# Kernel tuning notes

Measured on AMD Instinct MI355X. Metric: run time of the kernel, lower is better.

## Reference

```python
import jax, jax.numpy as jnp
import numpy as np

S, E, H, D, F = 2048, 1280, 16, 80, 5120
EPS = 1e-6


def _ln(x, g, b):
    m = x.mean(-1, keepdims=True)
    v = x.var(-1, keepdims=True)
    return (x - m) * jax.lax.rsqrt(v + EPS) * g + b


def _rotate_half(x):
    x1, x2 = jnp.split(x, 2, axis=-1)
    return jnp.concatenate([-x2, x1], axis=-1)


def _quick_gelu(x):
    return x * jax.nn.sigmoid(1.702 * x)


def setup_inputs() -> dict:
    key = jax.random.key(0)
    ks = jax.random.split(key, 12)
    inp = {
        "hidden_states": jax.random.normal(ks[0], (S, E), jnp.float32),
        "attention_mask": jnp.ones((1, 1, S, S), jnp.bool_),
        "cos": jax.random.uniform(ks[1], (S, D), jnp.float32),
        "sin": jax.random.uniform(ks[2], (S, D), jnp.float32),
        "ln1_g": jnp.ones((E,), jnp.float32),
        "ln1_b": jnp.zeros((E,), jnp.float32),
        "ln2_g": jnp.ones((E,), jnp.float32),
        "ln2_b": jnp.zeros((E,), jnp.float32),
        "w_qkv": jax.random.normal(ks[3], (E, 3 * E), jnp.float32) * (E ** -0.5),
        "b_qkv": jax.random.normal(ks[4], (3 * E,), jnp.float32) * 0.02,
        "w_o": jax.random.normal(ks[5], (E, E), jnp.float32) * (E ** -0.5),
        "b_o": jax.random.normal(ks[6], (E,), jnp.float32) * 0.02,
        "w_fc1": jax.random.normal(ks[7], (E, F), jnp.float32) * (E ** -0.5),
        "b_fc1": jax.random.normal(ks[8], (F,), jnp.float32) * 0.02,
        "w_fc2": jax.random.normal(ks[9], (F, E), jnp.float32) * (F ** -0.5),
        "b_fc2": jax.random.normal(ks[10], (E,), jnp.float32) * 0.02,
    }
    return inp


def reference(hidden_states, attention_mask, cos, sin, ln1_g, ln1_b, ln2_g, ln2_b,
              w_qkv, b_qkv, w_o, b_o, w_fc1, b_fc1, w_fc2, b_fc2):
    x = hidden_states  # [S, E]
    h = _ln(x, ln1_g, ln1_b)
    qkv = h @ w_qkv + b_qkv  # [S, 3E]
    q, k, v = jnp.split(qkv, 3, axis=-1)
    q = q.reshape(S, H, D)
    k = k.reshape(S, H, D)
    v = v.reshape(S, H, D)
    # rotary in fp32, cos/sin broadcast over head axis: [S, 1, D]
    c = cos[:, None, :].astype(jnp.float32)
    s = sin[:, None, :].astype(jnp.float32)
    qf, kf = q.astype(jnp.float32), k.astype(jnp.float32)
    q = (qf * c + _rotate_half(qf) * s).astype(q.dtype)
    k = (kf * c + _rotate_half(kf) * s).astype(k.dtype)
    # attention scores [H, S, S]
    scores = jnp.einsum('shd,thd->hst', q, k) / np.float32(np.sqrt(D))
    scores = jnp.where(attention_mask[0], scores, jnp.finfo(scores.dtype).min)
    probs = jax.nn.softmax(scores.astype(jnp.float32), axis=-1).astype(q.dtype)
    attn = jnp.einsum('hst,thd->shd', probs, v).reshape(S, E)
    attn = attn @ w_o + b_o
    x = x + attn
    h2 = _ln(x, ln2_g, ln2_b)
    mlp = _quick_gelu(h2 @ w_fc1 + b_fc1) @ w_fc2 + b_fc2
    return x + mlp
```

## Files before the change

kernel.cpp:

```cpp
#include <hip/hip_runtime.h>
#include <stdint.h>
#include <math.h>

#define S_LEN 2048
#define EMB   1280
#define NHEAD 16
#define HDIM  80
#define FDIM  5120

typedef __bf16 bf16x8 __attribute__((ext_vector_type(8)));
typedef float  f32x4  __attribute__((ext_vector_type(4)));
typedef int    i32x4  __attribute__((ext_vector_type(4)));
typedef unsigned short u16x8 __attribute__((ext_vector_type(8)));
typedef unsigned short u16x4 __attribute__((ext_vector_type(4)));

__device__ __forceinline__ float b2f(unsigned short u) {
    union { float f; unsigned int i; } x; x.i = ((unsigned int)u) << 16; return x.f;
}
__device__ __forceinline__ unsigned short f2b(float f) {
    union { float f; unsigned int i; } x; x.f = f;
    unsigned int r = x.i + 0x7FFFu + ((x.i >> 16) & 1u);
    return (unsigned short)(r >> 16);
}

__device__ __forceinline__ float wave_rsum(float v) {
    #pragma unroll
    for (int o = 32; o; o >>= 1) v += __shfl_down(v, o);
    return v;
}

__device__ __forceinline__ void trans64(
    const float* __restrict__ in, unsigned short* __restrict__ out,
    int R, int C, int bx, int by, int tid)
{
    __shared__ unsigned short tile[64][68];
    int c0 = bx * 64, r0 = by * 64;
    #pragma unroll
    for (int p = 0; p < 4; ++p) {
        int row  = p * 16 + (tid >> 4);
        int col4 = (tid & 15) * 4;
        f32x4 v = *(const f32x4*)&in[(size_t)(r0 + row) * C + c0 + col4];
        u16x4 b;
        #pragma unroll
        for (int j = 0; j < 4; ++j) b[j] = f2b(v[j]);
        *(u16x4*)&tile[row][col4] = b;
    }
    __syncthreads();
    #pragma unroll
    for (int p = 0; p < 4; ++p) {
        int orow = p * 16 + (tid >> 4);
        int oc4  = (tid & 15) * 4;
        u16x4 v;
        #pragma unroll
        for (int j = 0; j < 4; ++j) v[j] = tile[oc4 + j][orow];
        *(u16x4*)&out[(size_t)(c0 + orow) * R + r0 + oc4] = v;
    }
}

__global__ __launch_bounds__(256) void transpose4_kernel(
    const float* __restrict__ w_qkv, unsigned short* __restrict__ wT_qkv,
    const float* __restrict__ w_o,   unsigned short* __restrict__ wT_o,
    const float* __restrict__ w_fc1, unsigned short* __restrict__ wT_fc1,
    const float* __restrict__ w_fc2, unsigned short* __restrict__ wT_fc2)
{
    int id = blockIdx.x, tid = threadIdx.x;
    if (id < 1200) {
        trans64(w_qkv, wT_qkv, 1280, 3840, id % 60, id / 60, tid);
    } else if (id < 1600) {
        int t = id - 1200;
        trans64(w_o, wT_o, 1280, 1280, t % 20, t / 20, tid);
    } else if (id < 3200) {
        int t = id - 1600;
        trans64(w_fc1, wT_fc1, 1280, 5120, t % 80, t / 80, tid);
    } else {
        int t = id - 3200;
        trans64(w_fc2, wT_fc2, 5120, 1280, t % 20, t / 20, tid);
    }
}

__global__ __launch_bounds__(256) void ln_kernel(
    const float* __restrict__ x,
    const float* __restrict__ g,
    const float* __restrict__ b,
    unsigned short* __restrict__ out)
{
    int row = blockIdx.x, tid = threadIdx.x;
    int lane = tid & 63, wave = tid >> 6;
    const float* xr = x + (size_t)row * EMB;
    float v[5], s = 0.f, ss = 0.f;
    #pragma unroll
    for (int i = 0; i < 5; ++i) {
        float f = xr[tid + i * 256];
        v[i] = f; s += f; ss += f * f;
    }
    s = wave_rsum(s); ss = wave_rsum(ss);
    __shared__ float rs[4], rss[4];
    if (lane == 0) { rs[wave] = s; rss[wave] = ss; }
    __syncthreads();
    float st  = rs[0] + rs[1] + rs[2] + rs[3];
    float sst = rss[0] + rss[1] + rss[2] + rss[3];
    float mean = st * (1.0f / EMB);
    float var  = sst * (1.0f / EMB) - mean * mean;
    float inv  = rsqrtf(var + 1e-6f);
    unsigned short* orow = out + (size_t)row * EMB;
    #pragma unroll
    for (int i = 0; i < 5; ++i) {
        int c = tid + i * 256;
        orow[c] = f2b((v[i] - mean) * inv * g[c] + b[c]);
    }
}

__global__ __launch_bounds__(256) void reduce2ln_kernel(
    const float* __restrict__ part,
    const float* __restrict__ res,
    const float* __restrict__ bias,
    const float* __restrict__ g,
    const float* __restrict__ b,
    float* __restrict__ x_out,
    unsigned short* __restrict__ h_out)
{
    int row = blockIdx.x, tid = threadIdx.x;
    int lane = tid & 63, wave = tid >> 6;
    const size_t slice = (size_t)S_LEN * EMB;
    const float* p0 = part + (size_t)row * EMB;
    const float* p1 = p0 + slice;
    const float* rr = res + (size_t)row * EMB;
    float v[5], s = 0.f, ss = 0.f;
    #pragma unroll
    for (int i = 0; i < 5; ++i) {
        int c = tid + i * 256;
        float f = rr[c] + bias[c] + p0[c] + p1[c];
        v[i] = f; s += f; ss += f * f;
    }
    s = wave_rsum(s); ss = wave_rsum(ss);
    __shared__ float rs[4], rss[4];
    if (lane == 0) { rs[wave] = s; rss[wave] = ss; }
    __syncthreads();
    float st  = rs[0] + rs[1] + rs[2] + rs[3];
    float sst = rss[0] + rss[1] + rss[2] + rss[3];
    float mean = st * (1.0f / EMB);
    float var  = sst * (1.0f / EMB) - mean * mean;
    float inv  = rsqrtf(var + 1e-6f);
    float* xrow = x_out + (size_t)row * EMB;
    unsigned short* hrow = h_out + (size_t)row * EMB;
    #pragma unroll
    for (int i = 0; i < 5; ++i) {
        int c = tid + i * 256;
        xrow[c] = v[i];
        hrow[c] = f2b((v[i] - mean) * inv * g[c] + b[c]);
    }
}

template<int Z>
__global__ __launch_bounds__(256) void reduceZ_kernel(
    const float* __restrict__ part,
    const float* __restrict__ res,
    const float* __restrict__ bias,
    float* __restrict__ out)
{
    size_t i4 = ((size_t)blockIdx.x * 256 + threadIdx.x) * 4;
    int colb = (int)(i4 % EMB);
    f32x4 a = *(const f32x4*)&res[i4];
    f32x4 bv = *(const f32x4*)&bias[colb];
    a += bv;
    const size_t slice = (size_t)S_LEN * EMB;
    #pragma unroll
    for (int z = 0; z < Z; ++z)
        a += *(const f32x4*)&part[z * slice + i4];
    *(f32x4*)&out[i4] = a;
}

template<int EPI, int OM, int SPLIT, int BN>
__global__ __launch_bounds__(256) void gemm_kernel(
    const unsigned short* __restrict__ A,
    const unsigned short* __restrict__ Bt,
    const float* __restrict__ bias,
    void* __restrict__ Cv,
    int M, int N, int K)
{
    constexpr int NI = BN / 32;
    constexpr bool BX = (BN > 128);
    __shared__ __align__(16) unsigned short As[2][128 * 32];
    __shared__ __align__(16) unsigned short Bs[2][BN * 32];

    int tid = threadIdx.x;
    int lane = tid & 63, wave = tid >> 6;

    int gx = gridDim.x, gy = gridDim.y;
    int nwg = gx * gy * gridDim.z;
    int flat = blockIdx.x + gx * (blockIdx.y + gy * blockIdx.z);
    int cpx = nwg >> 3;
    int logical = (flat & 7) * cpx + (flat >> 3);
    int bx = logical % gx;
    int rem = logical / gx;
    int by = rem % gy;
    int bz = rem / gy;

    int m0 = bx * 128, n0 = by * BN;
    int wm = (wave >> 1) * 64, wn = (wave & 1) * (BN / 2);
    int kc = K / SPLIT;
    int kbeg = bz * kc;
    const int NITER = kc / 32;

    f32x4 acc[4][NI];
    #pragma unroll
    for (int i = 0; i < 4; ++i)
        #pragma unroll
        for (int j = 0; j < NI; ++j)
            acc[i][j] = (f32x4){0.f, 0.f, 0.f, 0.f};

    int u = tid ^ ((tid >> 3) & 7);
    const unsigned short* Ap0 = A  + (size_t)(m0 + (u >> 2)) * K + (u & 3) * 8 + kbeg;
    const unsigned short* Ap1 = Ap0 + (size_t)64 * K;
    const unsigned short* Bp0 = Bt + (size_t)(n0 + (u >> 2)) * K + (u & 3) * 8 + kbeg;
    const unsigned short* Bp1 = Bp0 + (size_t)64 * K;
    const unsigned short* Bp2 = Bp0 + (size_t)128 * K;
    const bool bxe = BX && (tid < 128);

    int arow = lane & 15, aq = (lane >> 4) * 8;
    int aswz = ((arow >> 1) & 7) << 3;
    int aoff[4], boff[NI];
    #pragma unroll
    for (int i = 0; i < 4; ++i)
        aoff[i] = ((wm + i * 16 + arow) * 32 + aq) ^ aswz;
    #pragma unroll
    for (int i = 0; i < NI; ++i)
        boff[i] = ((wn + i * 16 + arow) * 32 + aq) ^ aswz;

    i32x4 rA0a, rA1a, rB0a, rB1a, rB2a, rA0b, rA1b, rB0b, rB1b, rB2b;

    rA0b = *(const i32x4*)(Ap0);
    rA1b = *(const i32x4*)(Ap1);
    rB0b = *(const i32x4*)(Bp0);
    rB1b = *(const i32x4*)(Bp1);
    if (bxe) rB2b = *(const i32x4*)(Bp2);
    *(i32x4*)&As[0][tid * 8]        = rA0b;
    *(i32x4*)&As[0][2048 + tid * 8] = rA1b;
    *(i32x4*)&Bs[0][tid * 8]        = rB0b;
    *(i32x4*)&Bs[0][2048 + tid * 8] = rB1b;
    if (bxe) *(i32x4*)&Bs[0][4096 + tid * 8] = rB2b;
    if (NITER > 1) {
        rA0a = *(const i32x4*)(Ap0 + 32);
        rA1a = *(const i32x4*)(Ap1 + 32);
        rB0a = *(const i32x4*)(Bp0 + 32);
        rB1a = *(const i32x4*)(Bp1 + 32);
        if (bxe) rB2a = *(const i32x4*)(Bp2 + 32);
    }
    __syncthreads();

#define GSTEP(IT, AW0, AW1, BW0, BW1, BW2, AL0, AL1, BL0, BL1, BL2)          \
    {                                                                         \
        const int cur = (IT) & 1, nb = cur ^ 1;                               \
        if ((IT) + 1 < NITER) {                                               \
            *(i32x4*)&As[nb][tid * 8]        = AW0;                           \
            *(i32x4*)&As[nb][2048 + tid * 8] = AW1;                           \
            *(i32x4*)&Bs[nb][tid * 8]        = BW0;                           \
            *(i32x4*)&Bs[nb][2048 + tid * 8] = BW1;                           \
            if (bxe) *(i32x4*)&Bs[nb][4096 + tid * 8] = BW2;                  \
        }                                                                     \
        if ((IT) + 2 < NITER) {                                               \
            int ko = ((IT) + 2) * 32;                                         \
            AL0 = *(const i32x4*)(Ap0 + ko);                                  \
            AL1 = *(const i32x4*)(Ap1 + ko);                                  \
            BL0 = *(const i32x4*)(Bp0 + ko);                                  \
            BL1 = *(const i32x4*)(Bp1 + ko);                                  \
            if (bxe) BL2 = *(const i32x4*)(Bp2 + ko);                         \
        }                                                                     \
        bf16x8 af[4], bfm[NI];                                                \
        _Pragma("unroll") for (int i = 0; i < 4; ++i)                         \
            af[i]  = *(const bf16x8*)&As[cur][aoff[i]];                       \
        _Pragma("unroll") for (int i = 0; i < NI; ++i)                        \
            bfm[i] = *(const bf16x8*)&Bs[cur][boff[i]];                       \
        _Pragma("unroll") for (int mi = 0; mi < 4; ++mi)                      \
            _Pragma("unroll") for (int ni = 0; ni < NI; ++ni)                 \
                acc[mi][ni] = __builtin_amdgcn_mfma_f32_16x16x32_bf16(        \
                    af[mi], bfm[ni], acc[mi][ni], 0, 0, 0);                   \
        __syncthreads();                                                      \
    }

    for (int it = 0; it < NITER; it += 2) {
        GSTEP(it,     rA0a, rA1a, rB0a, rB1a, rB2a, rA0b, rA1b, rB0b, rB1b, rB2b)
        GSTEP(it + 1, rA0b, rA1b, rB0b, rB1b, rB2b, rA0a, rA1a, rB0a, rB1a, rB2a)
    }
#undef GSTEP

    int col = lane & 15;
    int rbase = (lane >> 4) * 4;
    #pragma unroll
    for (int ni = 0; ni < NI; ++ni) {
        int gn = n0 + wn + ni * 16 + col;
        float bv = (OM == 2) ? 0.f : bias[gn];
        #pragma unroll
        for (int mi = 0; mi < 4; ++mi) {
            int gm = m0 + wm + mi * 16 + rbase;
            #pragma unroll
            for (int r = 0; r < 4; ++r) {
                float v = acc[mi][ni][r] + bv;
                if (OM != 2) {
                    if (EPI == 1) v = v / (1.0f + expf(-1.702f * v));
                }
                if (OM == 2)
                    ((float*)Cv)[((size_t)bz * M + gm + r) * N + gn] = v;
                else
                    ((unsigned short*)Cv)[(size_t)(gm + r) * N + gn] = f2b(v);
            }
        }
    }
}

__global__ __launch_bounds__(256) void ropev_kernel(
    const unsigned short* __restrict__ qkv,
    const float* __restrict__ cosb,
    const float* __restrict__ sinb,
    unsigned short* __restrict__ q_out,
    unsigned short* __restrict__ k_out,
    unsigned short* __restrict__ vt)
{
    __shared__ unsigned short qT[64 * 84];
    __shared__ unsigned short kT[64 * 84];
    __shared__ unsigned short vT[64 * 84];

    int h = blockIdx.x >> 5, stile = blockIdx.x & 31;
    int s0 = stile * 64;
    int tid = threadIdx.x;

    u16x4 qr[5], kr[5];
    #pragma unroll
    for (int i = 0; i < 5; ++i) {
        int u = tid + i * 256;
        int row = u / 20, col = (u % 20) * 4;
        const unsigned short* base = qkv + (size_t)(s0 + row) * (3 * EMB) + h * HDIM + col;
        qr[i] = *(const u16x4*)base;
        kr[i] = *(const u16x4*)(base + EMB);
        u16x4 v4 = *(const u16x4*)(base + 2 * EMB);
        *(u16x4*)&qT[row * 84 + col] = qr[i];
        *(u16x4*)&kT[row * 84 + col] = kr[i];
        *(u16x4*)&vT[row * 84 + col] = v4;
    }
    __syncthreads();

    #pragma unroll
    for (int i = 0; i < 5; ++i) {
        int u = tid + i * 256;
        int row = u / 20, col = (u % 20) * 4;
        int pcol = (col < 40) ? col + 40 : col - 40;
        float sgn = (col < 40) ? -1.f : 1.f;
        u16x4 qp = *(const u16x4*)&qT[row * 84 + pcol];
        u16x4 kp = *(const u16x4*)&kT[row * 84 + pcol];
        f32x4 c4 = *(const f32x4*)&cosb[(size_t)(s0 + row) * HDIM + col];
        f32x4 s4 = *(const f32x4*)&sinb[(size_t)(s0 + row) * HDIM + col];
        u16x4 qo, ko;
        #pragma unroll
        for (int j = 0; j < 4; ++j) {
            qo[j] = f2b(b2f(qr[i][j]) * c4[j] + sgn * b2f(qp[j]) * s4[j]);
            ko[j] = f2b(b2f(kr[i][j]) * c4[j] + sgn * b2f(kp[j]) * s4[j]);
        }
        size_t o = ((size_t)h * S_LEN + s0 + row) * HDIM + col;
        *(u16x4*)&q_out[o] = qo;
        *(u16x4*)&k_out[o] = ko;
    }
    #pragma unroll
    for (int i = 0; i < 5; ++i) {
        int w = tid + i * 256;
        int d = w >> 4, c4i = (w & 15) * 4;
        u16x4 pk;
        #pragma unroll
        for (int j = 0; j < 4; ++j) pk[j] = vT[(c4i + j) * 84 + d];
        *(u16x4*)(vt + ((size_t)h * HDIM + d) * S_LEN + s0 + c4i) = pk;
    }
}

__global__ __launch_bounds__(256) void fattn_kernel(
    const unsigned short* __restrict__ q,
    const unsigned short* __restrict__ k,
    const unsigned short* __restrict__ vt,
    unsigned short* __restrict__ out)
{
    __shared__ __align__(16) unsigned short Ks[2][64 * 96];
    __shared__ __align__(16) unsigned short Vs[3][80 * 72];
    __shared__ __align__(16) unsigned short Pt[4 * 16 * 72];

    int tid = threadIdx.x;
    int lane = tid & 63, wave = tid >> 6;
    int arow = lane & 15, quad = lane >> 4;
    int logical = (blockIdx.x & 7) * 64 + (blockIdx.x >> 3);
    int h = logical >> 5, qb = logical & 31;
    int s0 = qb * 64;
    const float c = 0.16129856f;

    const unsigned short* kbase = k + (size_t)h * S_LEN * HDIM;
    const unsigned short* vbase = vt + (size_t)h * HDIM * S_LEN;

    bf16x8 qf[3];
    {
        const unsigned short* qrp =
            q + ((size_t)h * S_LEN + s0 + wave * 16 + arow) * HDIM;
        #pragma unroll
        for (int kk = 0; kk < 3; ++kk) {
            int col = kk * 32 + quad * 8;
            u16x8 qv = (u16x8){0, 0, 0, 0, 0, 0, 0, 0};
            if (col < HDIM) qv = *(const u16x8*)(qrp + col);
            u16x8 qs8;
            #pragma unroll
            for (int j = 0; j < 8; ++j) qs8[j] = f2b(b2f(qv[j]) * c);
            qf[kk] = *(bf16x8*)&qs8;
        }
    }

    {
        int zr = tid >> 2, zc = 80 + (tid & 3) * 4;
        int zidx = (zr * 96 + zc) ^ ((zr & 7) << 3);
        *(u16x4*)&Ks[0][zidx] = (u16x4){0, 0, 0, 0};
        *(u16x4*)&Ks[1][zidx] = (u16x4){0, 0, 0, 0};
    }

    u16x4 kreg[5], vreg[5];
    #pragma unroll
    for (int i = 0; i < 5; ++i) {
        int u = tid + i * 256;
        kreg[i] = *(const u16x4*)(kbase + u * 4);
        vreg[i] = *(const u16x4*)(vbase + (size_t)(u >> 4) * S_LEN + (u & 15) * 4);
    }
    #pragma unroll
    for (int i = 0; i < 5; ++i) {
        int u = tid + i * 256;
        int row = u / 20, c4 = (u % 20) * 4;
        *(u16x4*)&Ks[0][(row * 96 + c4) ^ ((row & 7) << 3)] = kreg[i];
        *(u16x4*)&Vs[0][(u >> 4) * 72 + (u & 15) * 4] = vreg[i];
    }
    #pragma unroll
    for (int i = 0; i < 5; ++i) {
        int u = tid + i * 256;
        kreg[i] = *(const u16x4*)(kbase + (size_t)64 * HDIM + u * 4);
        vreg[i] = *(const u16x4*)(vbase + (size_t)(u >> 4) * S_LEN + 64 + (u & 15) * 4);
    }
    __syncthreads();

    int ksw[3];
    #pragma unroll
    for (int kk = 0; kk < 3; ++kk)
        ksw[kk] = (arow * 96 + kk * 32 + quad * 8) ^ ((arow & 7) << 3);

    int pw = wave * 16 * 72;
    int poff = pw + arow * 72 + ((arow >> 3) << 2);

    float l_part = 0.f;
    f32x4 o[5];
    #pragma unroll
    for (int di = 0; di < 5; ++di) o[di] = (f32x4){0.f, 0.f, 0.f, 0.f};

    const int NIT = S_LEN / 64;
    int vcur = 0;
    for (int it = 0; it < NIT; ++it) {
        int kcur = it & 1;
        int vnext = (vcur + 1 == 3) ? 0 : vcur + 1;
        int vprev = (vcur == 0) ? 2 : vcur - 1;
        if (it + 1 < NIT) {
            #pragma unroll
            for (int i = 0; i < 5; ++i) {
                int u = tid + i * 256;
                int row = u / 20, c4 = (u % 20) * 4;
                *(u16x4*)&Ks[kcur ^ 1][(row * 96 + c4) ^ ((row & 7) << 3)] = kreg[i];
                *(u16x4*)&Vs[vnext][(u >> 4) * 72 + (u & 15) * 4] = vreg[i];
            }
        }
        if (it + 2 < NIT) {
            int t0 = (it + 2) * 64;
            #pragma unroll
            for (int i = 0; i < 5; ++i) {
                int u = tid + i * 256;
                kreg[i] = *(const u16x4*)(kbase + (size_t)t0 * HDIM + u * 4);
                vreg[i] = *(const u16x4*)(vbase + (size_t)(u >> 4) * S_LEN + t0 + (u & 15) * 4);
            }
        }

        __builtin_amdgcn_s_setprio(1);
        f32x4 sc[4];
        #pragma unroll
        for (int ni = 0; ni < 4; ++ni) sc[ni] = (f32x4){0.f, 0.f, 0.f, 0.f};
        #pragma unroll
        for (int kk = 0; kk < 3; ++kk) {
            bf16x8 bq = qf[kk];
            #pragma unroll
            for (int ni = 0; ni < 4; ++ni) {
                bf16x8 ak = *(const bf16x8*)&Ks[kcur][ksw[kk] + ni * 1536];
                sc[ni] = __builtin_amdgcn_mfma_f32_16x16x32_bf16(ak, bq, sc[ni], 0, 0, 0);
            }
        }

        if (it > 0) {
            #pragma unroll
            for (int kk = 0; kk < 2; ++kk) {
                u16x4 plo = *(const u16x4*)&Pt[poff + kk * 32 + quad * 8];
                u16x4 phi = *(const u16x4*)&Pt[poff + kk * 32 + quad * 8 + 4];
                u16x8 apu = (u16x8){plo[0], plo[1], plo[2], plo[3],
                                    phi[0], phi[1], phi[2], phi[3]};
                bf16x8 ap = *(bf16x8*)&apu;
                #pragma unroll
                for (int di = 0; di < 5; ++di) {
                    bf16x8 bv = *(const bf16x8*)&Vs[vprev][(di * 16 + arow) * 72 + kk * 32 + quad * 8];
                    o[di] = __builtin_amdgcn_mfma_f32_16x16x32_bf16(ap, bv, o[di], 0, 0, 0);
                }
            }
        }
        __builtin_amdgcn_s_setprio(0);

        #pragma unroll
        for (int ni = 0; ni < 4; ++ni) {
            u16x4 pk;
            #pragma unroll
            for (int r = 0; r < 4; ++r) {
                float p = __builtin_amdgcn_exp2f(sc[ni][r]);
                l_part += p;
                __bf16 pb = (__bf16)p;
                pk[r] = *(unsigned short*)&pb;
            }
            *(u16x4*)&Pt[poff + ni * 16 + quad * 4] = pk;
        }

        __syncthreads();
        vcur = vnext;
    }

    {
        int vlast = (vcur == 0) ? 2 : vcur - 1;
        __builtin_amdgcn_s_setprio(1);
        #pragma unroll
        for (int kk = 0; kk < 2; ++kk) {
            u16x4 plo = *(const u16x4*)&Pt[poff + kk * 32 + quad * 8];
            u16x4 phi = *(const u16x4*)&Pt[poff + kk * 32 + quad * 8 + 4];
            u16x8 apu = (u16x8){plo[0], plo[1], plo[2], plo[3],
                                phi[0], phi[1], phi[2], phi[3]};
            bf16x8 ap = *(bf16x8*)&apu;
            #pragma unroll
            for (int di = 0; di < 5; ++di) {
                bf16x8 bv = *(const bf16x8*)&Vs[vlast][(di * 16 + arow) * 72 + kk * 32 + quad * 8];
                o[di] = __builtin_amdgcn_mfma_f32_16x16x32_bf16(ap, bv, o[di], 0, 0, 0);
            }
        }
        __builtin_amdgcn_s_setprio(0);
    }

    float l_run = l_part;
    l_run += __shfl_xor(l_run, 16);
    l_run += __shfl_xor(l_run, 32);

    float inv[4];
    #pragma unroll
    for (int r = 0; r < 4; ++r)
        inv[r] = 1.f / __shfl(l_run, (lane & 48) | (quad * 4 + r));
    #pragma unroll
    for (int r = 0; r < 4; ++r) {
        int gq = s0 + wave * 16 + quad * 4 + r;
        unsigned short* op = out + (size_t)gq * EMB + h * HDIM;
        #pragma unroll
        for (int di = 0; di < 5; ++di)
            op[di * 16 + arow] = f2b(o[di][r] * inv[r]);
    }
}

extern "C" void kernel_launch(void* const* d_in, const int* in_sizes, int n_in,
                              void* d_out, int out_size, void* d_ws, size_t ws_size,
                              hipStream_t stream)
{
    const float* hidden = (const float*)d_in[0];
    const float* cosb  = (const float*)d_in[2];
    const float* sinb  = (const float*)d_in[3];
    const float* ln1g  = (const float*)d_in[4];
    const float* ln1b  = (const float*)d_in[5];
    const float* ln2g  = (const float*)d_in[6];
    const float* ln2b  = (const float*)d_in[7];
    const float* w_qkv = (const float*)d_in[8];
    const float* b_qkv = (const float*)d_in[9];
    const float* w_o   = (const float*)d_in[10];
    const float* b_o   = (const float*)d_in[11];
    const float* w_fc1 = (const float*)d_in[12];
    const float* b_fc1 = (const float*)d_in[13];
    const float* w_fc2 = (const float*)d_in[14];
    const float* b_fc2 = (const float*)d_in[15];

    char* ws = (char*)d_ws;
    size_t off = 0;
    auto alloc = [&](size_t bytes) -> void* {
        void* p = (void*)(ws + off);
        off += (bytes + 255) & ~(size_t)255;
        return p;
    };
    unsigned short* wT_qkv = (unsigned short*)alloc((size_t)3840 * 1280 * 2);
    unsigned short* wT_o   = (unsigned short*)alloc((size_t)1280 * 1280 * 2);
    unsigned short* wT_fc1 = (unsigned short*)alloc((size_t)5120 * 1280 * 2);
    unsigned short* wT_fc2 = (unsigned short*)alloc((size_t)1280 * 5120 * 2);
    unsigned short* h1     = (unsigned short*)alloc((size_t)S_LEN * EMB * 2);
    unsigned short* qkv    = (unsigned short*)alloc((size_t)S_LEN * 3 * EMB * 2);
    unsigned short* q_r    = (unsigned short*)alloc((size_t)S_LEN * EMB * 2);
    unsigned short* k_r    = (unsigned short*)alloc((size_t)S_LEN * EMB * 2);
    unsigned short* vt_g   = (unsigned short*)alloc((size_t)S_LEN * EMB * 2);
    unsigned short* attn_o = (unsigned short*)alloc((size_t)S_LEN * EMB * 2);
    float*          x1     = (float*)alloc((size_t)S_LEN * EMB * 4);
    unsigned short* h2     = (unsigned short*)alloc((size_t)S_LEN * EMB * 2);
    unsigned short* mlp1   = (unsigned short*)alloc((size_t)S_LEN * FDIM * 2);
    float* partials = (float*)h1;

    transpose4_kernel<<<4800, 256, 0, stream>>>(
        w_qkv, wT_qkv, w_o, wT_o, w_fc1, wT_fc1, w_fc2, wT_fc2);

    ln_kernel<<<S_LEN, 256, 0, stream>>>(hidden, ln1g, ln1b, h1);

    gemm_kernel<0, 0, 1, 128><<<dim3(S_LEN / 128, 3840 / 128, 1), 256, 0, stream>>>(
        h1, wT_qkv, b_qkv, qkv, S_LEN, 3 * EMB, EMB);

    ropev_kernel<<<NHEAD * (S_LEN / 64), 256, 0, stream>>>(qkv, cosb, sinb, q_r, k_r, vt_g);

    fattn_kernel<<<NHEAD * (S_LEN / 64), 256, 0, stream>>>(q_r, k_r, vt_g, attn_o);

    gemm_kernel<0, 2, 2, 160><<<dim3(S_LEN / 128, 1280 / 160, 2), 256, 0, stream>>>(
        attn_o, wT_o, nullptr, partials, S_LEN, EMB, EMB);
    reduce2ln_kernel<<<S_LEN, 256, 0, stream>>>(
        partials, hidden, b_o, ln2g, ln2b, x1, h2);

    gemm_kernel<1, 0, 1, 160><<<dim3(S_LEN / 128, FDIM / 160, 1), 256, 0, stream>>>(
        h2, wT_fc1, b_fc1, mlp1, S_LEN, FDIM, EMB);

    gemm_kernel<0, 2, 4, 160><<<dim3(S_LEN / 128, 1280 / 160, 4), 256, 0, stream>>>(
        mlp1, wT_fc2, nullptr, partials, S_LEN, EMB, FDIM);
    reduceZ_kernel<4><<<(S_LEN * EMB / 4) / 256, 256, 0, stream>>>(
        partials, x1, b_fc2, (float*)d_out);
}
```

Baseline: 339.3 us.

## Fuse LN1 into weight prep and use 64-row GEMM tiles with less split-K

Merges the first layernorm into the weight-transpose launch, so one kernel launch and its tail are removed. Adds a BM template parameter to the GEMM so the out-projection and fc2 GEMMs can use 64x160 tiles. The fc2 split-K drops from 4 to 2, which halves the partial-sum traffic and the reduction work. Smaller M tiles lower per-block data reuse but keep the same or larger grid sizes.

```diff
diff --git a/kernel.cpp b/kernel.cpp
--- a/kernel.cpp
+++ b/kernel.cpp
@@ -57,11 +57,15 @@
     }
 }
 
-__global__ __launch_bounds__(256) void transpose4_kernel(
+__global__ __launch_bounds__(256) void prep_kernel(
     const float* __restrict__ w_qkv, unsigned short* __restrict__ wT_qkv,
     const float* __restrict__ w_o,   unsigned short* __restrict__ wT_o,
     const float* __restrict__ w_fc1, unsigned short* __restrict__ wT_fc1,
-    const float* __restrict__ w_fc2, unsigned short* __restrict__ wT_fc2)
+    const float* __restrict__ w_fc2, unsigned short* __restrict__ wT_fc2,
+    const float* __restrict__ x,
+    const float* __restrict__ g,
+    const float* __restrict__ b,
+    unsigned short* __restrict__ h_out)
 {
     int id = blockIdx.x, tid = threadIdx.x;
     if (id < 1200) {
@@ -72,41 +76,34 @@
     } else if (id < 3200) {
         int t = id - 1600;
         trans64(w_fc1, wT_fc1, 1280, 5120, t % 80, t / 80, tid);
-    } else {
+    } else if (id < 4800) {
         int t = id - 3200;
         trans64(w_fc2, wT_fc2, 5120, 1280, t % 20, t / 20, tid);
-    }
-}
-
-__global__ __launch_bounds__(256) void ln_kernel(
-    const float* __restrict__ x,
-    const float* __restrict__ g,
-    const float* __restrict__ b,
-    unsigned short* __restrict__ out)
-{
-    int row = blockIdx.x, tid = threadIdx.x;
-    int lane = tid & 63, wave = tid >> 6;
-    const float* xr = x + (size_t)row * EMB;
-    float v[5], s = 0.f, ss = 0.f;
-    #pragma unroll
-    for (int i = 0; i < 5; ++i) {
-        float f = xr[tid + i * 256];
-        v[i] = f; s += f; ss += f * f;
-    }
-    s = wave_rsum(s); ss = wave_rsum(ss);
-    __shared__ float rs[4], rss[4];
-    if (lane == 0) { rs[wave] = s; rss[wave] = ss; }
-    __syncthreads();
-    float st  = rs[0] + rs[1] + rs[2] + rs[3];
-    float sst = rss[0] + rss[1] + rss[2] + rss[3];
-    float mean = st * (1.0f / EMB);
-    float var  = sst * (1.0f / EMB) - mean * mean;
-    float inv  = rsqrtf(var + 1e-6f);
-    unsigned short* orow = out + (size_t)row * EMB;
-    #pragma unroll
-    for (int i = 0; i < 5; ++i) {
-        int c = tid + i * 256;
-        orow[c] = f2b((v[i] - mean) * inv * g[c] + b[c]);
+    } else {
+        int row = id - 4800;
+        int lane = tid & 63, wave = tid >> 6;
+        const float* xr = x + (size_t)row * EMB;
+        float v[5], s = 0.f, ss = 0.f;
+        #pragma unroll
+        for (int i = 0; i < 5; ++i) {
+            float f = xr[tid + i * 256];
+            v[i] = f; s += f; ss += f * f;
+        }
+        s = wave_rsum(s); ss = wave_rsum(ss);
+        __shared__ float rs[4], rss[4];
+        if (lane == 0) { rs[wave] = s; rss[wave] = ss; }
+        __syncthreads();
+        float st  = rs[0] + rs[1] + rs[2] + rs[3];
+        float sst = rss[0] + rss[1] + rss[2] + rss[3];
+        float mean = st * (1.0f / EMB);
+        float var  = sst * (1.0f / EMB) - mean * mean;
+        float inv  = rsqrtf(var + 1e-6f);
+        unsigned short* orow = h_out + (size_t)row * EMB;
+        #pragma unroll
+        for (int i = 0; i < 5; ++i) {
+            int c = tid + i * 256;
+            orow[c] = f2b((v[i] - mean) * inv * g[c] + b[c]);
+        }
     }
 }
 
@@ -170,7 +167,7 @@
     *(f32x4*)&out[i4] = a;
 }
 
-template<int EPI, int OM, int SPLIT, int BN>
+template<int EPI, int OM, int SPLIT, int BM, int BN>
 __global__ __launch_bounds__(256) void gemm_kernel(
     const unsigned short* __restrict__ A,
     const unsigned short* __restrict__ Bt,
@@ -179,8 +176,10 @@
     int M, int N, int K)
 {
     constexpr int NI = BN / 32;
+    constexpr int MI = BM / 32;
     constexpr bool BX = (BN > 128);
-    __shared__ __align__(16) unsigned short As[2][128 * 32];
+    constexpr bool A2 = (BM > 64);
+    __shared__ __align__(16) unsigned short As[2][BM * 32];
     __shared__ __align__(16) unsigned short Bs[2][BN * 32];
 
     int tid = threadIdx.x;
@@ -196,15 +195,15 @@
     int by = rem % gy;
     int bz = rem / gy;
 
-    int m0 = bx * 128, n0 = by * BN;
-    int wm = (wave >> 1) * 64, wn = (wave & 1) * (BN / 2);
+    int m0 = bx * BM, n0 = by * BN;
+    int wm = (wave >> 1) * (BM / 2), wn = (wave & 1) * (BN / 2);
     int kc = K / SPLIT;
     int kbeg = bz * kc;
     const int NITER = kc / 32;
 
-    f32x4 acc[4][NI];
-    #pragma unroll
-    for (int i = 0; i < 4; ++i)
+    f32x4 acc[MI][NI];
+    #pragma unroll
+    for (int i = 0; i < MI; ++i)
         #pragma unroll
         for (int j = 0; j < NI; ++j)
             acc[i][j] = (f32x4){0.f, 0.f, 0.f, 0.f};
@@ -219,9 +218,9 @@
 
     int arow = lane & 15, aq = (lane >> 4) * 8;
     int aswz = ((arow >> 1) & 7) << 3;
-    int aoff[4], boff[NI];
-    #pragma unroll
-    for (int i = 0; i < 4; ++i)
+    int aoff[MI], boff[NI];
+    #pragma unroll
+    for (int i = 0; i < MI; ++i)
         aoff[i] = ((wm + i * 16 + arow) * 32 + aq) ^ aswz;
     #pragma unroll
     for (int i = 0; i < NI; ++i)
@@ -230,18 +229,18 @@
     i32x4 rA0a, rA1a, rB0a, rB1a, rB2a, rA0b, rA1b, rB0b, rB1b, rB2b;
 
     rA0b = *(const i32x4*)(Ap0);
-    rA1b = *(const i32x4*)(Ap1);
+    if (A2) rA1b = *(const i32x4*)(Ap1);
     rB0b = *(const i32x4*)(Bp0);
     rB1b = *(const i32x4*)(Bp1);
     if (bxe) rB2b = *(const i32x4*)(Bp2);
-    *(i32x4*)&As[0][tid * 8]        = rA0b;
-    *(i32x4*)&As[0][2048 + tid * 8] = rA1b;
+    *(i32x4*)&As[0][tid * 8] = rA0b;
+    if (A2) *(i32x4*)&As[0][BM * 16 + tid * 8] = rA1b;
     *(i32x4*)&Bs[0][tid * 8]        = rB0b;
     *(i32x4*)&Bs[0][2048 + tid * 8] = rB1b;
     if (bxe) *(i32x4*)&Bs[0][4096 + tid * 8] = rB2b;
     if (NITER > 1) {
         rA0a = *(const i32x4*)(Ap0 + 32);
-        rA1a = *(const i32x4*)(Ap1 + 32);
+        if (A2) rA1a = *(const i32x4*)(Ap1 + 32);
         rB0a = *(const i32x4*)(Bp0 + 32);
         rB1a = *(const i32x4*)(Bp1 + 32);
         if (bxe) rB2a = *(const i32x4*)(Bp2 + 32);
@@ -252,8 +251,8 @@
     {                                                                         \
         const int cur = (IT) & 1, nb = cur ^ 1;                               \
         if ((IT) + 1 < NITER) {                                               \
-            *(i32x4*)&As[nb][tid * 8]        = AW0;                           \
-            *(i32x4*)&As[nb][2048 + tid * 8] = AW1;                           \
+            *(i32x4*)&As[nb][tid * 8] = AW0;                                  \
+            if (A2) *(i32x4*)&As[nb][BM * 16 + tid * 8] = AW1;                \
             *(i32x4*)&Bs[nb][tid * 8]        = BW0;                           \
             *(i32x4*)&Bs[nb][2048 + tid * 8] = BW1;                           \
             if (bxe) *(i32x4*)&Bs[nb][4096 + tid * 8] = BW2;                  \
@@ -261,17 +260,17 @@
         if ((IT) + 2 < NITER) {                                               \
             int ko = ((IT) + 2) * 32;                                         \
             AL0 = *(const i32x4*)(Ap0 + ko);                                  \
-            AL1 = *(const i32x4*)(Ap1 + ko);                                  \
+            if (A2) AL1 = *(const i32x4*)(Ap1 + ko);                          \
             BL0 = *(const i32x4*)(Bp0 + ko);                                  \
             BL1 = *(const i32x4*)(Bp1 + ko);                                  \
             if (bxe) BL2 = *(const i32x4*)(Bp2 + ko);                         \
         }                                                                     \
-        bf16x8 af[4], bfm[NI];                                                \
-        _Pragma("unroll") for (int i = 0; i < 4; ++i)                         \
+        bf16x8 af[MI], bfm[NI];                                               \
+        _Pragma("unroll") for (int i = 0; i < MI; ++i)                        \
             af[i]  = *(const bf16x8*)&As[cur][aoff[i]];                       \
         _Pragma("unroll") for (int i = 0; i < NI; ++i)                        \
             bfm[i] = *(const bf16x8*)&Bs[cur][boff[i]];                       \
-        _Pragma("unroll") for (int mi = 0; mi < 4; ++mi)                      \
+        _Pragma("unroll") for (int mi = 0; mi < MI; ++mi)                     \
             _Pragma("unroll") for (int ni = 0; ni < NI; ++ni)                 \
                 acc[mi][ni] = __builtin_amdgcn_mfma_f32_16x16x32_bf16(        \
                     af[mi], bfm[ni], acc[mi][ni], 0, 0, 0);                   \
@@ -291,7 +290,7 @@
         int gn = n0 + wn + ni * 16 + col;
         float bv = (OM == 2) ? 0.f : bias[gn];
         #pragma unroll
-        for (int mi = 0; mi < 4; ++mi) {
+        for (int mi = 0; mi < MI; ++mi) {
             int gm = m0 + wm + mi * 16 + rbase;
             #pragma unroll
             for (int r = 0; r < 4; ++r) {
@@ -601,28 +600,27 @@
     unsigned short* mlp1   = (unsigned short*)alloc((size_t)S_LEN * FDIM * 2);
     float* partials = (float*)h1;
 
-    transpose4_kernel<<<4800, 256, 0, stream>>>(
-        w_qkv, wT_qkv, w_o, wT_o, w_fc1, wT_fc1, w_fc2, wT_fc2);
-
-    ln_kernel<<<S_LEN, 256, 0, stream>>>(hidden, ln1g, ln1b, h1);
-
-    gemm_kernel<0, 0, 1, 128><<<dim3(S_LEN / 128, 3840 / 128, 1), 256, 0, stream>>>(
+    prep_kernel<<<4800 + S_LEN, 256, 0, stream>>>(
+        w_qkv, wT_qkv, w_o, wT_o, w_fc1, wT_fc1, w_fc2, wT_fc2,
+        hidden, ln1g, ln1b, h1);
+
+    gemm_kernel<0, 0, 1, 128, 128><<<dim3(S_LEN / 128, 3840 / 128, 1), 256, 0, stream>>>(
         h1, wT_qkv, b_qkv, qkv, S_LEN, 3 * EMB, EMB);
 
     ropev_kernel<<<NHEAD * (S_LEN / 64), 256, 0, stream>>>(qkv, cosb, sinb, q_r, k_r, vt_g);
 
     fattn_kernel<<<NHEAD * (S_LEN / 64), 256, 0, stream>>>(q_r, k_r, vt_g, attn_o);
 
-    gemm_kernel<0, 2, 2, 160><<<dim3(S_LEN / 128, 1280 / 160, 2), 256, 0, stream>>>(
+    gemm_kernel<0, 2, 2, 64, 160><<<dim3(S_LEN / 64, 1280 / 160, 2), 256, 0, stream>>>(
         attn_o, wT_o, nullptr, partials, S_LEN, EMB, EMB);
     reduce2ln_kernel<<<S_LEN, 256, 0, stream>>>(
         partials, hidden, b_o, ln2g, ln2b, x1, h2);
 
-    gemm_kernel<1, 0, 1, 160><<<dim3(S_LEN / 128, FDIM / 160, 1), 256, 0, stream>>>(
+    gemm_kernel<1, 0, 1, 128, 160><<<dim3(S_LEN / 128, FDIM / 160, 1), 256, 0, stream>>>(
         h2, wT_fc1, b_fc1, mlp1, S_LEN, FDIM, EMB);
 
-    gemm_kernel<0, 2, 4, 160><<<dim3(S_LEN / 128, 1280 / 160, 4), 256, 0, stream>>>(
+    gemm_kernel<0, 2, 2, 64, 160><<<dim3(S_LEN / 64, 1280 / 160, 2), 256, 0, stream>>>(
         mlp1, wT_fc2, nullptr, partials, S_LEN, EMB, FDIM);
-    reduceZ_kernel<4><<<(S_LEN * EMB / 4) / 256, 256, 0, stream>>>(
+    reduceZ_kernel<2><<<(S_LEN * EMB / 4) / 256, 256, 0, stream>>>(
         partials, x1, b_fc2, (float*)d_out);
 }
```

Result: no change. 345.1 us (+1.7%).
